# Performance work log

Measured on AMD Instinct MI355X. Metric: run time of the kernel, lower is better.

Reference implementation:

```python
import jax, jax.numpy as jnp
import numpy as np

N_HEADS = 16
MASK_VAL = -50000.0  # module sets masked scores to this value (not -inf)


def setup_inputs() -> dict:
    key = jax.random.key(0)
    kq, kk, kv = jax.random.split(key, 3)
    b, n, d_model = 2, 2048, 2048
    q = jax.random.normal(kq, (b, n, d_model), dtype=jnp.float32)
    k = jax.random.normal(kk, (b, n, d_model), dtype=jnp.float32)
    v = jax.random.normal(kv, (b, n, d_model), dtype=jnp.float32)
    return {"q": q, "k": k, "v": v}


def reference(q, k, v):
    b, n, d_model = q.shape
    h = N_HEADS
    dh = d_model // h
    scale = dh ** -0.5
    # 'b n (h d) -> b h n d'
    qh = q.reshape(b, n, h, dh).transpose(0, 2, 1, 3)
    kh = k.reshape(b, n, h, dh).transpose(0, 2, 1, 3)
    vh = v.reshape(b, n, h, dh).transpose(0, 2, 1, 3)
    # dots = (q * scale) @ k^T  -> [b, h, n, n]
    dots = jnp.einsum('bhid,bhjd->bhij', qh * scale, kh)
    # per-chunk triu_indices(csz, l, offset=i*csz+1) == global causal mask j > i,
    # with masked entries SET to MASK_VAL
    i_idx = jnp.arange(n)[:, None]
    j_idx = jnp.arange(n)[None, :]
    dots = jnp.where(j_idx > i_idx, MASK_VAL, dots)
    attn = jax.nn.softmax(dots, axis=-1)
    out = jnp.einsum('bhij,bhjd->bhid', attn, vh)
    # 'b h n d -> b n (h d)'
    return out.transpose(0, 2, 1, 3).reshape(b, n, d_model)
```

## Files before the change

kernel.cpp:

```cpp
#include <hip/hip_runtime.h>
#include <hip/hip_bf16.h>

#define B_SZ   2
#define N_SEQ  2048
#define NH     16
#define DH     128
#define DM     2048
#define QB     128
#define KVB    64
#define NQT    (N_SEQ / QB)
#define MASK_VAL (-50000.0f)

typedef short bf16x8 __attribute__((ext_vector_type(8)));
typedef float f32x4  __attribute__((ext_vector_type(4)));
typedef float f32x16 __attribute__((ext_vector_type(16)));
typedef unsigned u32;
typedef unsigned u32x2 __attribute__((ext_vector_type(2)));
typedef unsigned u32x4 __attribute__((ext_vector_type(4)));
typedef unsigned short ushort_t;

__device__ __forceinline__ u32 pk2(float a, float b) {
  u32 r;
  asm("v_cvt_pk_bf16_f32 %0, %1, %2" : "=v"(r) : "v"(a), "v"(b));
  return r;
}

__device__ __forceinline__ void gload_lds16(const void* g, void* l) {
  __builtin_amdgcn_global_load_lds(
      (const __attribute__((address_space(1))) unsigned int*)g,
      (__attribute__((address_space(3))) unsigned int*)l, 16, 0, 0);
}

__global__ __launch_bounds__(256)
void kconv(const float* __restrict__ k, ushort_t* __restrict__ kw) {
  const int idx = blockIdx.x * 256 + threadIdx.x;
  const size_t e0 = (size_t)idx * 16;
  const int c0 = (int)(e0 & 2047);
  const int bn = (int)(e0 >> 11);
  const int b  = bn >> 11;
  const int n  = bn & 2047;
  const int h  = c0 >> 7;
  const int d0 = c0 & 127;
  const float* src = k + e0;
  float4 f0 = *(const float4*)(src);
  float4 f1 = *(const float4*)(src + 4);
  float4 f2 = *(const float4*)(src + 8);
  float4 f3 = *(const float4*)(src + 12);
  u32x4 p0, p1;
  p0[0] = pk2(f0.x, f0.y); p0[1] = pk2(f0.z, f0.w);
  p0[2] = pk2(f1.x, f1.y); p0[3] = pk2(f1.z, f1.w);
  p1[0] = pk2(f2.x, f2.y); p1[1] = pk2(f2.z, f2.w);
  p1[2] = pk2(f3.x, f3.y); p1[3] = pk2(f3.z, f3.w);
  ushort_t* dst = kw + (((size_t)(b * 16 + h) * 2048 + n) * 128 + d0);
  *(u32x4*)(dst)     = p0;
  *(u32x4*)(dst + 8) = p1;
}

__global__ __launch_bounds__(256)
void vtrans(const float* __restrict__ v, ushort_t* __restrict__ vw) {
  __shared__ __align__(16) char tile[16384];

  const int tid   = threadIdx.x;
  const int bid   = blockIdx.x;
  const int ntile = bid & 31;
  const int bh2   = bid >> 5;
  const int h     = bh2 & 15;
  const int n0    = ntile * 64;
  const float* vbase = v + (size_t)(bh2 >> 4) * N_SEQ * DM + h * DH;

  #pragma unroll
  for (int i = 0; i < 8; ++i) {
    int idx = i * 256 + tid;
    int n   = idx >> 5;
    int c4  = idx & 31;
    float4 f = *(const float4*)(vbase + (size_t)(n0 + n) * DM + c4 * 4);
    u32x2 p;
    p[0] = pk2(f.x, f.y);
    p[1] = pk2(f.z, f.w);
    int sw = (((n & 7) ^ (n >> 3)) << 4);
    *(u32x2*)(tile + n * 256 + ((8 * c4) ^ sw)) = p;
  }
  __syncthreads();

  #pragma unroll
  for (int i = 0; i < 4; ++i) {
    int idx = i * 256 + tid;
    int d   = idx >> 3;
    int nb  = idx & 7;
    u32x4 p;
    #pragma unroll
    for (int half = 0; half < 4; ++half) {
      int na = nb * 8 + half * 2;
      int nA = na, nB = na + 1;
      int swA = (((nA & 7) ^ (nA >> 3)) << 4);
      int swB = (((nB & 7) ^ (nB >> 3)) << 4);
      u32 lo = *(const ushort_t*)(tile + nA * 256 + (((d >> 2) * 8) ^ swA) + (d & 3) * 2);
      u32 hi = *(const ushort_t*)(tile + nB * 256 + (((d >> 2) * 8) ^ swB) + (d & 3) * 2);
      p[half] = lo | (hi << 16);
    }
    ushort_t* dst = vw + (((size_t)bh2 * 128 + d) * 2048 + n0 + nb * 8);
    *(u32x4*)(dst) = p;
  }
}

__global__ __launch_bounds__(256, 2)
void attn_fwd(const float* __restrict__ q, const ushort_t* __restrict__ kw,
              const ushort_t* __restrict__ vw, float* __restrict__ out) {
  __shared__ __align__(16) char  ldsK[64 * 256];
  __shared__ __align__(16) char  ldsVT[128 * 128];
  __shared__ __align__(16) float ldsA[4 * 32];

  const int tid  = threadIdx.x;
  const int lane = tid & 63;
  const int w    = tid >> 6;
  const int h    = lane >> 5;
  const int il   = lane & 31;

  const int bid = blockIdx.x;
  const int bh  = bid & 31;
  const int qt  = (bid < 256) ? (bid >> 5) : (NQT - 1 - ((bid - 256) >> 5));
  const int b   = bh >> 4;
  const int hd  = bh & 15;
  const int q0  = qt * QB;
  const int wq0 = q0 + w * 32;
  const int irow = wq0 + il;

  const float scale = 0.08838834764831845f;

  const ushort_t* kb16 = kw + (size_t)(b * 16 + hd) * N_SEQ * DH;
  const ushort_t* vt16 = vw + (size_t)(b * 16 + hd) * DH * N_SEQ;

  bf16x8 qf[8];
  {
    const float* qr = q + ((size_t)b * N_SEQ + irow) * DM + hd * DH + h * 8;
    #pragma unroll
    for (int s = 0; s < 8; ++s) {
      float4 a = *(const float4*)(qr + s * 16);
      float4 c = *(const float4*)(qr + s * 16 + 4);
      u32x4 t4;
      t4[0] = pk2(a.x * scale, a.y * scale);
      t4[1] = pk2(a.z * scale, a.w * scale);
      t4[2] = pk2(c.x * scale, c.y * scale);
      t4[3] = pk2(c.z * scale, c.w * scale);
      qf[s] = __builtin_bit_cast(bf16x8, t4);
    }
  }

  float m_ = -INFINITY, ll = 0.f;
  f32x16 o[4];
  #pragma unroll
  for (int dt = 0; dt < 4; ++dt)
    #pragma unroll
    for (int r = 0; r < 16; ++r) o[dt][r] = 0.f;

  const int kswz = (il & 7) << 4;
  const int nt = 2 * qt + 2;

  const int krL = lane >> 4;
  const int kpL = lane & 15;
  const int vdL = lane >> 3;
  const int vcL = lane & 7;

  for (int t = 0; t < nt; ++t) {
    const int jt = t * KVB;
    if (t) __syncthreads();

    {
      const ushort_t* kt = kb16 + (size_t)jt * DH;
      #pragma unroll
      for (int c = 0; c < 4; ++c) {
        const int base = (w * 4 + c) * 1024;
        const int r    = (w * 4 + c) * 4 + krL;
        const ushort_t* g = kt + (size_t)r * DH + ((kpL ^ (r & 7)) * 8);
        gload_lds16(g, ldsK + base);
      }
      #pragma unroll
      for (int c = 0; c < 4; ++c) {
        const int base = (w * 4 + c) * 1024;
        const int d    = (w * 4 + c) * 8 + vdL;
        const ushort_t* g = vt16 + (size_t)d * N_SEQ + jt + ((vcL ^ (d & 7)) * 8);
        gload_lds16(g, ldsVT + base);
      }
    }
    __syncthreads();

    if (jt > wq0 + 31) continue;
    const bool act1 = (jt + 32 <= wq0 + 31);

    f32x16 sc0 = {0,0,0,0,0,0,0,0,0,0,0,0,0,0,0,0};
    f32x16 sc1 = {0,0,0,0,0,0,0,0,0,0,0,0,0,0,0,0};
    __builtin_amdgcn_s_setprio(1);
    #pragma unroll
    for (int s = 0; s < 8; ++s) {
      bf16x8 kf0 = *(const bf16x8*)(ldsK + il * 256 + ((s * 32 + h * 16) ^ kswz));
      sc0 = __builtin_amdgcn_mfma_f32_32x32x16_bf16(kf0, qf[s], sc0, 0, 0, 0);
    }
    if (act1) {
      #pragma unroll
      for (int s = 0; s < 8; ++s) {
        bf16x8 kf1 = *(const bf16x8*)(ldsK + (32 + il) * 256 + ((s * 32 + h * 16) ^ kswz));
        sc1 = __builtin_amdgcn_mfma_f32_32x32x16_bf16(kf1, qf[s], sc1, 0, 0, 0);
      }
    }
    __builtin_amdgcn_s_setprio(0);

    if (jt + 31 > wq0) {
      #pragma unroll
      for (int r = 0; r < 16; ++r) {
        int j = jt + (r & 3) + 8 * (r >> 2) + 4 * h;
        sc0[r] = (j > irow) ? MASK_VAL : sc0[r];
      }
    }
    if (act1 && (jt + 63 > wq0)) {
      #pragma unroll
      for (int r = 0; r < 16; ++r) {
        int j = jt + 32 + (r & 3) + 8 * (r >> 2) + 4 * h;
        sc1[r] = (j > irow) ? MASK_VAL : sc1[r];
      }
    }

    float pmax = sc0[0];
    #pragma unroll
    for (int r = 1; r < 16; ++r) pmax = fmaxf(pmax, sc0[r]);
    if (act1) {
      #pragma unroll
      for (int r = 0; r < 16; ++r) pmax = fmaxf(pmax, sc1[r]);
    }
    pmax = fmaxf(pmax, __shfl_xor(pmax, 32));

    if (!__all(pmax <= m_ + 8.f)) {
      const float mnew = fmaxf(m_, pmax);
      const float alpha = __expf(m_ - mnew);
      ll *= alpha;
      m_ = mnew;
      ldsA[w * 32 + il] = alpha;
      f32x4 av[4];
      #pragma unroll
      for (int m = 0; m < 4; ++m)
        av[m] = *(const f32x4*)(ldsA + w * 32 + 8 * m + 4 * h);
      #pragma unroll
      for (int dt = 0; dt < 4; ++dt)
        #pragma unroll
        for (int m = 0; m < 4; ++m)
          #pragma unroll
          for (int r2 = 0; r2 < 4; ++r2)
            o[dt][m * 4 + r2] *= av[m][r2];
    }

    #pragma unroll
    for (int r = 0; r < 16; ++r) sc0[r] = __expf(sc0[r] - m_);
    if (act1) {
      #pragma unroll
      for (int r = 0; r < 16; ++r) sc1[r] = __expf(sc1[r] - m_);
    }
    float rs = 0.f;
    #pragma unroll
    for (int r = 0; r < 16; ++r) rs += sc0[r];
    if (act1) {
      #pragma unroll
      for (int r = 0; r < 16; ++r) rs += sc1[r];
    }
    rs += __shfl_xor(rs, 32);
    ll += rs;

    bf16x8 pa0[2], pa1[2];
    #pragma unroll
    for (int ss = 0; ss < 2; ++ss) {
      u32 w0 = pk2(sc0[8 * ss + 0], sc0[8 * ss + 1]);
      u32 w1 = pk2(sc0[8 * ss + 2], sc0[8 * ss + 3]);
      u32 w2 = pk2(sc0[8 * ss + 4], sc0[8 * ss + 5]);
      u32 w3 = pk2(sc0[8 * ss + 6], sc0[8 * ss + 7]);
      asm volatile("v_permlane32_swap_b32 %0, %1" : "+v"(w0), "+v"(w2));
      asm volatile("v_permlane32_swap_b32 %0, %1" : "+v"(w1), "+v"(w3));
      u32x4 t4 = {w0, w1, w2, w3};
      pa0[ss] = __builtin_bit_cast(bf16x8, t4);
    }
    if (act1) {
      #pragma unroll
      for (int ss = 0; ss < 2; ++ss) {
        u32 w0 = pk2(sc1[8 * ss + 0], sc1[8 * ss + 1]);
        u32 w1 = pk2(sc1[8 * ss + 2], sc1[8 * ss + 3]);
        u32 w2 = pk2(sc1[8 * ss + 4], sc1[8 * ss + 5]);
        u32 w3 = pk2(sc1[8 * ss + 6], sc1[8 * ss + 7]);
        asm volatile("v_permlane32_swap_b32 %0, %1" : "+v"(w0), "+v"(w2));
        asm volatile("v_permlane32_swap_b32 %0, %1" : "+v"(w1), "+v"(w3));
        u32x4 t4 = {w0, w1, w2, w3};
        pa1[ss] = __builtin_bit_cast(bf16x8, t4);
      }
    }

    __builtin_amdgcn_s_setprio(1);
    #pragma unroll
    for (int dt = 0; dt < 4; ++dt) {
      const int drow = dt * 32 + il;
      char* vrow = ldsVT + drow * 128;
      bf16x8 vf0 = *(const bf16x8*)(vrow + ((0 * 32 + 16 * h) ^ kswz));
      o[dt] = __builtin_amdgcn_mfma_f32_32x32x16_bf16(pa0[0], vf0, o[dt], 0, 0, 0);
      bf16x8 vf1 = *(const bf16x8*)(vrow + ((1 * 32 + 16 * h) ^ kswz));
      o[dt] = __builtin_amdgcn_mfma_f32_32x32x16_bf16(pa0[1], vf1, o[dt], 0, 0, 0);
      if (act1) {
        bf16x8 vf2 = *(const bf16x8*)(vrow + ((2 * 32 + 16 * h) ^ kswz));
        o[dt] = __builtin_amdgcn_mfma_f32_32x32x16_bf16(pa1[0], vf2, o[dt], 0, 0, 0);
        bf16x8 vf3 = *(const bf16x8*)(vrow + ((3 * 32 + 16 * h) ^ kswz));
        o[dt] = __builtin_amdgcn_mfma_f32_32x32x16_bf16(pa1[1], vf3, o[dt], 0, 0, 0);
      }
    }
    __builtin_amdgcn_s_setprio(0);
  }

  ldsA[w * 32 + il] = 1.0f / ll;
  f32x4 iv[4];
  #pragma unroll
  for (int m = 0; m < 4; ++m)
    iv[m] = *(const f32x4*)(ldsA + w * 32 + 8 * m + 4 * h);

  float* ob = out + ((size_t)b * N_SEQ + wq0) * DM + hd * DH;
  #pragma unroll
  for (int dt = 0; dt < 4; ++dt) {
    #pragma unroll
    for (int m = 0; m < 4; ++m) {
      #pragma unroll
      for (int r2 = 0; r2 < 4; ++r2) {
        int i_loc = 8 * m + 4 * h + r2;
        ob[(size_t)i_loc * DM + dt * 32 + il] = o[dt][m * 4 + r2] * iv[m][r2];
      }
    }
  }
}

extern "C" void kernel_launch(void* const* d_in, const int* in_sizes, int n_in,
                              void* d_out, int out_size, void* d_ws, size_t ws_size,
                              hipStream_t stream) {
  const float* q = (const float*)d_in[0];
  const float* k = (const float*)d_in[1];
  const float* v = (const float*)d_in[2];
  float* out = (float*)d_out;

  ushort_t* kw = (ushort_t*)d_ws;
  ushort_t* vw = kw + (size_t)B_SZ * NH * N_SEQ * DH;

  kconv <<<2048, 256, 0, stream>>>(k, kw);
  vtrans<<<1024, 256, 0, stream>>>(v, vw);
  attn_fwd<<<B_SZ * NH * NQT, 256, 0, stream>>>(q, kw, vw, out);
}
```

Before: 90.56 us.

## Double-buffer K/V tiles in LDS to overlap prefetch with compute

Doubles the K and V^T LDS buffers and issues the global-to-LDS loads for the next KV tile before computing on the current one. A single barrier per iteration replaces the load-then-barrier pattern, so global memory latency is meant to hide behind the MFMA and softmax work. The row max and row sum reductions also become tree reductions to shorten the serial dependency chain. LDS use per block grows to about 64KB, which puts pressure on the two-blocks-per-CU occupancy target.

```diff
diff --git a/kernel.cpp b/kernel.cpp
--- a/kernel.cpp
+++ b/kernel.cpp
@@ -29,6 +29,23 @@
   __builtin_amdgcn_global_load_lds(
       (const __attribute__((address_space(1))) unsigned int*)g,
       (__attribute__((address_space(3))) unsigned int*)l, 16, 0, 0);
+}
+
+__device__ __forceinline__ float tmax16(const f32x16& v) {
+  float a = fmaxf(v[0], v[1]),  b = fmaxf(v[2], v[3]);
+  float c = fmaxf(v[4], v[5]),  d = fmaxf(v[6], v[7]);
+  float e = fmaxf(v[8], v[9]),  f = fmaxf(v[10], v[11]);
+  float g = fmaxf(v[12], v[13]), h = fmaxf(v[14], v[15]);
+  a = fmaxf(a, b); c = fmaxf(c, d); e = fmaxf(e, f); g = fmaxf(g, h);
+  return fmaxf(fmaxf(a, c), fmaxf(e, g));
+}
+__device__ __forceinline__ float tsum16(const f32x16& v) {
+  float a = v[0] + v[1],  b = v[2] + v[3];
+  float c = v[4] + v[5],  d = v[6] + v[7];
+  float e = v[8] + v[9],  f = v[10] + v[11];
+  float g = v[12] + v[13], h = v[14] + v[15];
+  a += b; c += d; e += f; g += h;
+  return (a + c) + (e + g);
 }
 
 __global__ __launch_bounds__(256)
@@ -106,8 +123,8 @@
 __global__ __launch_bounds__(256, 2)
 void attn_fwd(const float* __restrict__ q, const ushort_t* __restrict__ kw,
               const ushort_t* __restrict__ vw, float* __restrict__ out) {
-  __shared__ __align__(16) char  ldsK[64 * 256];
-  __shared__ __align__(16) char  ldsVT[128 * 128];
+  __shared__ __align__(16) char  ldsK[2 * 64 * 256];
+  __shared__ __align__(16) char  ldsVT[2 * 128 * 128];
   __shared__ __align__(16) float ldsA[4 * 32];
 
   const int tid  = threadIdx.x;
@@ -129,6 +146,31 @@
 
   const ushort_t* kb16 = kw + (size_t)(b * 16 + hd) * N_SEQ * DH;
   const ushort_t* vt16 = vw + (size_t)(b * 16 + hd) * DH * N_SEQ;
+
+  const int krL = lane >> 4;
+  const int kpL = lane & 15;
+  const int vdL = lane >> 3;
+  const int vcL = lane & 7;
+
+  auto stage = [&](int jt, int buf) {
+    char* K  = ldsK  + buf * 16384;
+    char* VT = ldsVT + buf * 16384;
+    const ushort_t* kt = kb16 + (size_t)jt * DH;
+    #pragma unroll
+    for (int c = 0; c < 4; ++c) {
+      const int base = (w * 4 + c) * 1024;
+      const int r    = (w * 4 + c) * 4 + krL;
+      const ushort_t* g = kt + (size_t)r * DH + ((kpL ^ (r & 7)) * 8);
+      gload_lds16(g, K + base);
+    }
+    #pragma unroll
+    for (int c = 0; c < 4; ++c) {
+      const int base = (w * 4 + c) * 1024;
+      const int d    = (w * 4 + c) * 8 + vdL;
+      const ushort_t* g = vt16 + (size_t)d * N_SEQ + jt + ((vcL ^ (d & 7)) * 8);
+      gload_lds16(g, VT + base);
+    }
+  };
 
   bf16x8 qf[8];
   {
@@ -156,156 +198,131 @@
   const int kswz = (il & 7) << 4;
   const int nt = 2 * qt + 2;
 
-  const int krL = lane >> 4;
-  const int kpL = lane & 15;
-  const int vdL = lane >> 3;
-  const int vcL = lane & 7;
+  stage(0, 0);
+  __syncthreads();
 
   for (int t = 0; t < nt; ++t) {
-    const int jt = t * KVB;
-    if (t) __syncthreads();
-
-    {
-      const ushort_t* kt = kb16 + (size_t)jt * DH;
-      #pragma unroll
-      for (int c = 0; c < 4; ++c) {
-        const int base = (w * 4 + c) * 1024;
-        const int r    = (w * 4 + c) * 4 + krL;
-        const ushort_t* g = kt + (size_t)r * DH + ((kpL ^ (r & 7)) * 8);
-        gload_lds16(g, ldsK + base);
-      }
-      #pragma unroll
-      for (int c = 0; c < 4; ++c) {
-        const int base = (w * 4 + c) * 1024;
-        const int d    = (w * 4 + c) * 8 + vdL;
-        const ushort_t* g = vt16 + (size_t)d * N_SEQ + jt + ((vcL ^ (d & 7)) * 8);
-        gload_lds16(g, ldsVT + base);
-      }
-    }
-    __syncthreads();
-
-    if (jt > wq0 + 31) continue;
-    const bool act1 = (jt + 32 <= wq0 + 31);
-
-    f32x16 sc0 = {0,0,0,0,0,0,0,0,0,0,0,0,0,0,0,0};
-    f32x16 sc1 = {0,0,0,0,0,0,0,0,0,0,0,0,0,0,0,0};
-    __builtin_amdgcn_s_setprio(1);
-    #pragma unroll
-    for (int s = 0; s < 8; ++s) {
-      bf16x8 kf0 = *(const bf16x8*)(ldsK + il * 256 + ((s * 32 + h * 16) ^ kswz));
-      sc0 = __builtin_amdgcn_mfma_f32_32x32x16_bf16(kf0, qf[s], sc0, 0, 0, 0);
-    }
-    if (act1) {
+    const int jt  = t * KVB;
+    const int cur = t & 1;
+    if (t + 1 < nt) stage(jt + KVB, cur ^ 1);
+
+    if (jt <= wq0 + 31) {
+      char* K  = ldsK  + cur * 16384;
+      char* VT = ldsVT + cur * 16384;
+      const bool act1 = (jt + 32 <= wq0 + 31);
+
+      f32x16 sc0 = {0,0,0,0,0,0,0,0,0,0,0,0,0,0,0,0};
+      f32x16 sc1 = {0,0,0,0,0,0,0,0,0,0,0,0,0,0,0,0};
+      __builtin_amdgcn_s_setprio(1);
       #pragma unroll
       for (int s = 0; s < 8; ++s) {
-        bf16x8 kf1 = *(const bf16x8*)(ldsK + (32 + il) * 256 + ((s * 32 + h * 16) ^ kswz));
-        sc1 = __builtin_amdgcn_mfma_f32_32x32x16_bf16(kf1, qf[s], sc1, 0, 0, 0);
-      }
-    }
-    __builtin_amdgcn_s_setprio(0);
-
-    if (jt + 31 > wq0) {
-      #pragma unroll
-      for (int r = 0; r < 16; ++r) {
-        int j = jt + (r & 3) + 8 * (r >> 2) + 4 * h;
-        sc0[r] = (j > irow) ? MASK_VAL : sc0[r];
-      }
-    }
-    if (act1 && (jt + 63 > wq0)) {
-      #pragma unroll
-      for (int r = 0; r < 16; ++r) {
-        int j = jt + 32 + (r & 3) + 8 * (r >> 2) + 4 * h;
-        sc1[r] = (j > irow) ? MASK_VAL : sc1[r];
-      }
-    }
-
-    float pmax = sc0[0];
-    #pragma unroll
-    for (int r = 1; r < 16; ++r) pmax = fmaxf(pmax, sc0[r]);
-    if (act1) {
-      #pragma unroll
-      for (int r = 0; r < 16; ++r) pmax = fmaxf(pmax, sc1[r]);
-    }
-    pmax = fmaxf(pmax, __shfl_xor(pmax, 32));
-
-    if (!__all(pmax <= m_ + 8.f)) {
-      const float mnew = fmaxf(m_, pmax);
-      const float alpha = __expf(m_ - mnew);
-      ll *= alpha;
-      m_ = mnew;
-      ldsA[w * 32 + il] = alpha;
-      f32x4 av[4];
-      #pragma unroll
-      for (int m = 0; m < 4; ++m)
-        av[m] = *(const f32x4*)(ldsA + w * 32 + 8 * m + 4 * h);
-      #pragma unroll
-      for (int dt = 0; dt < 4; ++dt)
+        bf16x8 kf0 = *(const bf16x8*)(K + il * 256 + ((s * 32 + h * 16) ^ kswz));
+        sc0 = __builtin_amdgcn_mfma_f32_32x32x16_bf16(kf0, qf[s], sc0, 0, 0, 0);
+      }
+      if (act1) {
+        #pragma unroll
+        for (int s = 0; s < 8; ++s) {
+          bf16x8 kf1 = *(const bf16x8*)(K + (32 + il) * 256 + ((s * 32 + h * 16) ^ kswz));
+          sc1 = __builtin_amdgcn_mfma_f32_32x32x16_bf16(kf1, qf[s], sc1, 0, 0, 0);
+        }
+      }
+      __builtin_amdgcn_s_setprio(0);
+
+      if (jt + 31 > wq0) {
+        #pragma unroll
+        for (int r = 0; r < 16; ++r) {
+          int j = jt + (r & 3) + 8 * (r >> 2) + 4 * h;
+          sc0[r] = (j > irow) ? MASK_VAL : sc0[r];
+        }
+      }
+      if (act1 && (jt + 63 > wq0)) {
+        #pragma unroll
+        for (int r = 0; r < 16; ++r) {
+          int j = jt + 32 + (r & 3) + 8 * (r >> 2) + 4 * h;
+          sc1[r] = (j > irow) ? MASK_VAL : sc1[r];
+        }
+      }
+
+      float pmax = tmax16(sc0);
+      if (act1) pmax = fmaxf(pmax, tmax16(sc1));
+      pmax = fmaxf(pmax, __shfl_xor(pmax, 32));
+
+      if (!__all(pmax <= m_ + 8.f)) {
+        const float mnew = fmaxf(m_, pmax);
+        const float alpha = __expf(m_ - mnew);
+        ll *= alpha;
+        m_ = mnew;
+        ldsA[w * 32 + il] = alpha;
+        f32x4 av[4];
         #pragma unroll
         for (int m = 0; m < 4; ++m)
+          av[m] = *(const f32x4*)(ldsA + w * 32 + 8 * m + 4 * h);
+        #pragma unroll
+        for (int dt = 0; dt < 4; ++dt)
           #pragma unroll
-          for (int r2 = 0; r2 < 4; ++r2)
-            o[dt][m * 4 + r2] *= av[m][r2];
-    }
-
-    #pragma unroll
-    for (int r = 0; r < 16; ++r) sc0[r] = __expf(sc0[r] - m_);
-    if (act1) {
-      #pragma unroll
-      for (int r = 0; r < 16; ++r) sc1[r] = __expf(sc1[r] - m_);
-    }
-    float rs = 0.f;
-    #pragma unroll
-    for (int r = 0; r < 16; ++r) rs += sc0[r];
-    if (act1) {
-      #pragma unroll
-      for (int r = 0; r < 16; ++r) rs += sc1[r];
-    }
-    rs += __shfl_xor(rs, 32);
-    ll += rs;
-
-    bf16x8 pa0[2], pa1[2];
-    #pragma unroll
-    for (int ss = 0; ss < 2; ++ss) {
-      u32 w0 = pk2(sc0[8 * ss + 0], sc0[8 * ss + 1]);
-      u32 w1 = pk2(sc0[8 * ss + 2], sc0[8 * ss + 3]);
-      u32 w2 = pk2(sc0[8 * ss + 4], sc0[8 * ss + 5]);
-      u32 w3 = pk2(sc0[8 * ss + 6], sc0[8 * ss + 7]);
-      asm volatile("v_permlane32_swap_b32 %0, %1" : "+v"(w0), "+v"(w2));
-      asm volatile("v_permlane32_swap_b32 %0, %1" : "+v"(w1), "+v"(w3));
-      u32x4 t4 = {w0, w1, w2, w3};
-      pa0[ss] = __builtin_bit_cast(bf16x8, t4);
-    }
-    if (act1) {
+          for (int m = 0; m < 4; ++m)
+            #pragma unroll
+            for (int r2 = 0; r2 < 4; ++r2)
+              o[dt][m * 4 + r2] *= av[m][r2];
+      }
+
+      #pragma unroll
+      for (int r = 0; r < 16; ++r) sc0[r] = __expf(sc0[r] - m_);
+      if (act1) {
+        #pragma unroll
+        for (int r = 0; r < 16; ++r) sc1[r] = __expf(sc1[r] - m_);
+      }
+      float rs = tsum16(sc0);
+      if (act1) rs += tsum16(sc1);
+      rs += __shfl_xor(rs, 32);
+      ll += rs;
+
+      bf16x8 pa0[2], pa1[2];
       #pragma unroll
       for (int ss = 0; ss < 2; ++ss) {
-        u32 w0 = pk2(sc1[8 * ss + 0], sc1[8 * ss + 1]);
-        u32 w1 = pk2(sc1[8 * ss + 2], sc1[8 * ss + 3]);
-        u32 w2 = pk2(sc1[8 * ss + 4], sc1[8 * ss + 5]);
-        u32 w3 = pk2(sc1[8 * ss + 6], sc1[8 * ss + 7]);
+        u32 w0 = pk2(sc0[8 * ss + 0], sc0[8 * ss + 1]);
+        u32 w1 = pk2(sc0[8 * ss + 2], sc0[8 * ss + 3]);
+        u32 w2 = pk2(sc0[8 * ss + 4], sc0[8 * ss + 5]);
+        u32 w3 = pk2(sc0[8 * ss + 6], sc0[8 * ss + 7]);
         asm volatile("v_permlane32_swap_b32 %0, %1" : "+v"(w0), "+v"(w2));
         asm volatile("v_permlane32_swap_b32 %0, %1" : "+v"(w1), "+v"(w3));
         u32x4 t4 = {w0, w1, w2, w3};
-        pa1[ss] = __builtin_bit_cast(bf16x8, t4);
-      }
-    }
-
-    __builtin_amdgcn_s_setprio(1);
-    #pragma unroll
-    for (int dt = 0; dt < 4; ++dt) {
-      const int drow = dt * 32 + il;
-      char* vrow = ldsVT + drow * 128;
-      bf16x8 vf0 = *(const bf16x8*)(vrow + ((0 * 32 + 16 * h) ^ kswz));
-      o[dt] = __builtin_amdgcn_mfma_f32_32x32x16_bf16(pa0[0], vf0, o[dt], 0, 0, 0);
-      bf16x8 vf1 = *(const bf16x8*)(vrow + ((1 * 32 + 16 * h) ^ kswz));
-      o[dt] = __builtin_amdgcn_mfma_f32_32x32x16_bf16(pa0[1], vf1, o[dt], 0, 0, 0);
+        pa0[ss] = __builtin_bit_cast(bf16x8, t4);
+      }
       if (act1) {
-        bf16x8 vf2 = *(const bf16x8*)(vrow + ((2 * 32 + 16 * h) ^ kswz));
-        o[dt] = __builtin_amdgcn_mfma_f32_32x32x16_bf16(pa1[0], vf2, o[dt], 0, 0, 0);
-        bf16x8 vf3 = *(const bf16x8*)(vrow + ((3 * 32 + 16 * h) ^ kswz));
-        o[dt] = __builtin_amdgcn_mfma_f32_32x32x16_bf16(pa1[1], vf3, o[dt], 0, 0, 0);
-      }
-    }
-    __builtin_amdgcn_s_setprio(0);
+        #pragma unroll
+        for (int ss = 0; ss < 2; ++ss) {
+          u32 w0 = pk2(sc1[8 * ss + 0], sc1[8 * ss + 1]);
+          u32 w1 = pk2(sc1[8 * ss + 2], sc1[8 * ss + 3]);
+          u32 w2 = pk2(sc1[8 * ss + 4], sc1[8 * ss + 5]);
+          u32 w3 = pk2(sc1[8 * ss + 6], sc1[8 * ss + 7]);
+          asm volatile("v_permlane32_swap_b32 %0, %1" : "+v"(w0), "+v"(w2));
+          asm volatile("v_permlane32_swap_b32 %0, %1" : "+v"(w1), "+v"(w3));
+          u32x4 t4 = {w0, w1, w2, w3};
+          pa1[ss] = __builtin_bit_cast(bf16x8, t4);
+        }
+      }
+
+      __builtin_amdgcn_s_setprio(1);
+      #pragma unroll
+      for (int dt = 0; dt < 4; ++dt) {
+        const int drow = dt * 32 + il;
+        char* vrow = VT + drow * 128;
+        bf16x8 vf0 = *(const bf16x8*)(vrow + ((0 * 32 + 16 * h) ^ kswz));
+        o[dt] = __builtin_amdgcn_mfma_f32_32x32x16_bf16(pa0[0], vf0, o[dt], 0, 0, 0);
+        bf16x8 vf1 = *(const bf16x8*)(vrow + ((1 * 32 + 16 * h) ^ kswz));
+        o[dt] = __builtin_amdgcn_mfma_f32_32x32x16_bf16(pa0[1], vf1, o[dt], 0, 0, 0);
+        if (act1) {
+          bf16x8 vf2 = *(const bf16x8*)(vrow + ((2 * 32 + 16 * h) ^ kswz));
+          o[dt] = __builtin_amdgcn_mfma_f32_32x32x16_bf16(pa1[0], vf2, o[dt], 0, 0, 0);
+          bf16x8 vf3 = *(const bf16x8*)(vrow + ((3 * 32 + 16 * h) ^ kswz));
+          o[dt] = __builtin_amdgcn_mfma_f32_32x32x16_bf16(pa1[1], vf3, o[dt], 0, 0, 0);
+        }
+      }
+      __builtin_amdgcn_s_setprio(0);
+    }
+
+    if (t + 1 < nt) __syncthreads();
   }
 
   ldsA[w * 32 + il] = 1.0f / ll;
```

Result: slower. 93.91 us (+3.7%).
